# Performance work log

Hardware: AMD Instinct MI355X
Metric: run time of the kernel (lower is better)

The kernel has to match this reference:

```python
import jax, jax.numpy as jnp
import numpy as np

B, L = 1024, 50
H = 512
N_ITEM, N_ENTITY, N_WORD = 50000, 100000, 30000


def setup_inputs() -> dict:
    key = jax.random.key(0)
    ks = jax.random.split(key, 16)
    inp = {
        "item_ids": jax.random.randint(ks[0], (B, L), 0, N_ITEM),
        "item_len": jax.random.randint(ks[1], (B,), 0, 51),
        "entity_ids": jax.random.randint(ks[2], (B, L), 0, N_ENTITY),
        "entity_len": jax.random.randint(ks[3], (B,), 0, 51),
        "word_ids": jax.random.randint(ks[4], (B, L), 0, N_WORD),
        "word_len": jax.random.randint(ks[5], (B,), 0, 51),
        "labels": jax.random.randint(ks[6], (B,), 0, N_ITEM),
        # learned parameters (torch default-ish init scales)
        "item_emb": jax.random.normal(ks[7], (N_ITEM, H), jnp.float32),
        "entity_emb": jax.random.normal(ks[8], (N_ENTITY, H), jnp.float32),
        "word_emb": jax.random.normal(ks[9], (N_WORD, H), jnp.float32),
        "W1": jax.random.normal(ks[10], (H, 4 * H), jnp.float32) / np.sqrt(H),
        "b1": jnp.zeros((4 * H,), jnp.float32),
        "W2": jax.random.normal(ks[11], (4 * H, N_ITEM), jnp.float32) / np.sqrt(4 * H),
        "b2": jnp.zeros((N_ITEM,), jnp.float32),
    }
    return inp


def _masked_mean(table, ids, lens):
    # segment-mean over ragged lists encoded as padded ids + lengths.
    # empty list -> zeros (matches the torch zero-fallback branch).
    mask = (jnp.arange(L)[None, :] < lens[:, None]).astype(table.dtype)  # [B,L]
    emb = table[ids]                                                     # [B,L,H]
    s = jnp.einsum("blh,bl->bh", emb, mask)
    denom = jnp.maximum(lens, 1).astype(table.dtype)[:, None]
    return s / denom


def reference(item_emb, entity_emb, word_emb, W1, b1, W2, b2,
              item_ids, item_len, entity_ids, entity_len,
              word_ids, word_len, labels):
    u = (_masked_mean(item_emb, item_ids, item_len)
         + _masked_mean(entity_emb, entity_ids, entity_len)
         + _masked_mean(word_emb, word_ids, word_len)) / 3.0   # [B,H]
    h = jax.nn.relu(u @ W1 + b1)                                # [B,4H]
    probs = jax.nn.softmax(h @ W2 + b2, axis=-1)                # [B,n_item]
    # faithful to source: CrossEntropyLoss applied on top of softmax outputs
    logp = jax.nn.log_softmax(probs, axis=-1)
    loss = -jnp.mean(jnp.take_along_axis(logp, labels[:, None], axis=-1))
    return probs, labels, loss
```

## Files before the change

### kernel.cpp

```cpp
#include <hip/hip_runtime.h>
#include <cstdint>
#include <cstddef>

typedef __attribute__((ext_vector_type(8))) short bf16x8;
typedef __attribute__((ext_vector_type(4))) float f32x4;

#define B_DIM 1024
#define L_SEQ 50
#define H_DIM 512
#define NITEM 50000
#define PSTRIDE 400

__device__ __forceinline__ unsigned short f2bf(float x) {
  unsigned u = __float_as_uint(x);
  return (unsigned short)((u + 0x7fffu + ((u >> 16) & 1u)) >> 16);
}
__device__ __forceinline__ unsigned pack2(float lo, float hi) {
  return (unsigned)f2bf(lo) | ((unsigned)f2bf(hi) << 16);
}

__global__ void mean_kernel(const int* __restrict__ item_ids, const int* __restrict__ item_len,
                            const int* __restrict__ ent_ids, const int* __restrict__ ent_len,
                            const int* __restrict__ word_ids, const int* __restrict__ word_len,
                            const float* __restrict__ item_emb, const float* __restrict__ ent_emb,
                            const float* __restrict__ word_emb, unsigned short* __restrict__ u_bf) {
  const int b = blockIdx.x >> 1;
  const int col = ((blockIdx.x & 1) << 8) + threadIdx.x;
  float out = 0.f;
  {
    const int len = item_len[b]; float a = 0.f;
#pragma unroll 4
    for (int l = 0; l < len; ++l) a += item_emb[(size_t)item_ids[b * L_SEQ + l] * H_DIM + col];
    out += a / (float)(len > 0 ? len : 1);
  }
  {
    const int len = ent_len[b]; float a = 0.f;
#pragma unroll 4
    for (int l = 0; l < len; ++l) a += ent_emb[(size_t)ent_ids[b * L_SEQ + l] * H_DIM + col];
    out += a / (float)(len > 0 ? len : 1);
  }
  {
    const int len = word_len[b]; float a = 0.f;
#pragma unroll 4
    for (int l = 0; l < len; ++l) a += word_emb[(size_t)word_ids[b * L_SEQ + l] * H_DIM + col];
    out += a / (float)(len > 0 ? len : 1);
  }
  u_bf[b * H_DIM + col] = f2bf(out / 3.f);
}

template <int K, int N, int EPI>
__global__ __launch_bounds__(512, 2) void gemm_fused(const unsigned short* __restrict__ Ag,
                                                     const float* __restrict__ Bg,
                                                     const float* __restrict__ bias,
                                                     unsigned short* __restrict__ Cbf,
                                                     float* __restrict__ Cf,
                                                     float* __restrict__ pmax,
                                                     float* __restrict__ psum) {
  __shared__ unsigned short As[2][256 * 64];
  __shared__ uint4 Bs[2][8 * 128];

  const int tid = threadIdx.x;
  const int lane = tid & 63;
  const int wid = tid >> 6;
  const int m0 = blockIdx.x * 256;
  const int n0 = blockIdx.y * 128;

  const int arow = tid >> 3;
  const int ach = tid & 7;
  const int bn = 2 * lane;
  const int bk = 8 * wid;
  const int bcolg = (n0 + bn < N - 2) ? (n0 + bn) : (N - 2);

  uint4 areg[4];
  float2 breg[8];
  f32x4 acc[4][4] = {};

  auto stage_global = [&](int kt) {
    const int k0 = kt * 64;
#pragma unroll
    for (int q = 0; q < 4; ++q)
      areg[q] = *(const uint4*)&Ag[(size_t)(m0 + arow + 64 * q) * K + k0 + 8 * ach];
#pragma unroll
    for (int i = 0; i < 8; ++i)
      breg[i] = *(const float2*)&Bg[(size_t)(k0 + bk + i) * N + bcolg];
  };

  auto stage_lds = [&](int buf) {
#pragma unroll
    for (int q = 0; q < 4; ++q) {
      const int row = arow + 64 * q;
      *(uint4*)&As[buf][row * 64 + ((8 * ach) ^ ((row & 7) * 8))] = areg[q];
    }
    uint4 c0, c1;
    c0.x = pack2(breg[0].x, breg[1].x); c0.y = pack2(breg[2].x, breg[3].x);
    c0.z = pack2(breg[4].x, breg[5].x); c0.w = pack2(breg[6].x, breg[7].x);
    c1.x = pack2(breg[0].y, breg[1].y); c1.y = pack2(breg[2].y, breg[3].y);
    c1.z = pack2(breg[4].y, breg[5].y); c1.w = pack2(breg[6].y, breg[7].y);
    Bs[buf][wid * 128 + bn] = c0;
    Bs[buf][wid * 128 + bn + 1] = c1;
  };

  const int wr = wid & 3, wc = wid >> 2;
  const int mw = 64 * wr, nw = 64 * wc;
  const int l15 = lane & 15, kb = lane >> 4;

  auto compute = [&](int buf) {
#pragma unroll
    for (int koi = 0; koi < 2; ++koi) {
      bf16x8 af[4], bfv[4];
#pragma unroll
      for (int i = 0; i < 4; ++i) {
        const int row = mw + 16 * i + l15;
        af[i] = *(const bf16x8*)&As[buf][row * 64 + ((32 * koi + 8 * kb) ^ ((row & 7) * 8))];
      }
#pragma unroll
      for (int j = 0; j < 4; ++j)
        bfv[j] = *(const bf16x8*)&Bs[buf][(4 * koi + kb) * 128 + nw + 16 * j + l15];
#pragma unroll
      for (int i = 0; i < 4; ++i)
#pragma unroll
        for (int j = 0; j < 4; ++j)
          acc[i][j] = __builtin_amdgcn_mfma_f32_16x16x32_bf16(af[i], bfv[j], acc[i][j], 0, 0, 0);
    }
  };

  const int NT = K / 64;
  stage_global(0);
  stage_lds(0);
  __syncthreads();
  for (int t = 0; t < NT; ++t) {
    const int cur = t & 1;
    if (t + 1 < NT) stage_global(t + 1);
    compute(cur);
    if (t + 1 < NT) stage_lds(cur ^ 1);
    __syncthreads();
  }

  float bv[4];
  bool val[4];
#pragma unroll
  for (int j = 0; j < 4; ++j) {
    const int cg = n0 + nw + 16 * j + l15;
    val[j] = (cg < N);
    bv[j] = bias[val[j] ? cg : 0];
  }
#pragma unroll
  for (int i = 0; i < 4; ++i) {
    const int rbase = m0 + mw + 16 * i + 4 * kb;
#pragma unroll
    for (int j = 0; j < 4; ++j) {
      if (val[j]) {
        const int cg = n0 + nw + 16 * j + l15;
#pragma unroll
        for (int r = 0; r < 4; ++r) {
          const float v = acc[i][j][r] + bv[j];
          if (EPI == 0)
            Cbf[(size_t)(rbase + r) * N + cg] = f2bf(v > 0.f ? v : 0.f);
          else
            Cf[(size_t)(rbase + r) * N + cg] = v;
        }
      }
    }
  }

  if constexpr (EPI == 1) {
    float* redm = (float*)&As[0][0];
    float* reds = redm + 512;
#pragma unroll
    for (int i = 0; i < 4; ++i) {
#pragma unroll
      for (int r = 0; r < 4; ++r) {
        float mx = -3.0e38f;
#pragma unroll
        for (int j = 0; j < 4; ++j)
          if (val[j]) mx = fmaxf(mx, acc[i][j][r] + bv[j]);
#pragma unroll
        for (int d = 1; d < 16; d <<= 1) mx = fmaxf(mx, __shfl_xor(mx, d));
        float s = 0.f;
#pragma unroll
        for (int j = 0; j < 4; ++j)
          if (val[j]) s += expf(acc[i][j][r] + bv[j] - mx);
#pragma unroll
        for (int d = 1; d < 16; d <<= 1) s += __shfl_xor(s, d);
        if (l15 == 0) {
          const int rl = mw + 16 * i + 4 * kb + r;
          redm[wc * 256 + rl] = mx;
          reds[wc * 256 + rl] = s;
        }
      }
    }
    __syncthreads();
    if (tid < 256) {
      const float ma = redm[tid], mb = redm[256 + tid];
      const float mm = fmaxf(ma, mb);
      const float ss = reds[tid] * expf(ma - mm) + reds[256 + tid] * expf(mb - mm);
      pmax[(size_t)(m0 + tid) * PSTRIDE + blockIdx.y] = mm;
      psum[(size_t)(m0 + tid) * PSTRIDE + blockIdx.y] = ss;
    }
  }
}

__global__ void smax1r(const float* __restrict__ pmax, const float* __restrict__ psum,
                       float* __restrict__ rms, int ntiles) {
  const int b = blockIdx.x;
  const int l = threadIdx.x;
  float m = -3.4e38f, s = 0.f;
  for (int i = l; i < ntiles; i += 64) {
    const float pm = pmax[(size_t)b * PSTRIDE + i];
    const float ps = psum[(size_t)b * PSTRIDE + i];
    const float nm = fmaxf(m, pm);
    s = s * expf(m - nm) + ps * expf(pm - nm);
    m = nm;
  }
  for (int d = 1; d < 64; d <<= 1) {
    const float om = __shfl_xor(m, d), os = __shfl_xor(s, d);
    const float nm = fmaxf(m, om);
    s = s * expf(m - nm) + os * expf(om - nm);
    m = nm;
  }
  if (l == 0) {
    rms[b] = m;
    rms[B_DIM + b] = s;
  }
}

__global__ void smax2(float* __restrict__ buf, const float* __restrict__ rms,
                      const int* __restrict__ labels, float* __restrict__ row_lp) {
  const int b = blockIdx.x;
  float4* p = (float4*)(buf + (size_t)b * NITEM);
  const float m = rms[b];
  const float inv = 1.f / rms[B_DIM + b];
  const int lab = labels[b];
  __shared__ float s_pl;
  __shared__ float ss[256];
  float s2 = 0.f;
  for (int i = threadIdx.x; i < NITEM / 4; i += 256) {
    const float4 v = p[i];
    float pr[4];
#pragma unroll
    for (int j = 0; j < 4; ++j) {
      pr[j] = expf((&v.x)[j] - m) * inv;
      s2 += expf(pr[j] - inv);
    }
    float4 w;
    w.x = pr[0]; w.y = pr[1]; w.z = pr[2]; w.w = pr[3];
    p[i] = w;
    if ((lab >> 2) == i) s_pl = pr[lab & 3];
  }
  ss[threadIdx.x] = s2;
  __syncthreads();
  for (int off = 128; off > 0; off >>= 1) {
    if (threadIdx.x < off) ss[threadIdx.x] += ss[threadIdx.x + off];
    __syncthreads();
  }
  if (threadIdx.x == 0) row_lp[b] = s_pl - (inv + logf(ss[0]));
}

__global__ void fin(const float* __restrict__ row_lp, const int* __restrict__ labels,
                    float* __restrict__ out) {
  __shared__ float sb[256];
  float a = 0.f;
  for (int i = threadIdx.x; i < B_DIM; i += 256) {
    a += row_lp[i];
    out[(size_t)B_DIM * NITEM + i] = (float)labels[i];
  }
  sb[threadIdx.x] = a;
  __syncthreads();
  for (int off = 128; off > 0; off >>= 1) {
    if (threadIdx.x < off) sb[threadIdx.x] += sb[threadIdx.x + off];
    __syncthreads();
  }
  if (threadIdx.x == 0) out[(size_t)B_DIM * NITEM + B_DIM] = -sb[0] / (float)B_DIM;
}

extern "C" void kernel_launch(void* const* d_in, const int* in_sizes, int n_in,
                              void* d_out, int out_size, void* d_ws, size_t ws_size,
                              hipStream_t stream) {
  const int* item_ids = (const int*)d_in[0];
  const int* item_len = (const int*)d_in[1];
  const int* ent_ids = (const int*)d_in[2];
  const int* ent_len = (const int*)d_in[3];
  const int* word_ids = (const int*)d_in[4];
  const int* word_len = (const int*)d_in[5];
  const int* labels = (const int*)d_in[6];
  const float* item_emb = (const float*)d_in[7];
  const float* ent_emb = (const float*)d_in[8];
  const float* word_emb = (const float*)d_in[9];
  const float* W1 = (const float*)d_in[10];
  const float* b1 = (const float*)d_in[11];
  const float* W2 = (const float*)d_in[12];
  const float* b2 = (const float*)d_in[13];

  float* out = (float*)d_out;
  char* ws = (char*)d_ws;
  unsigned short* u_bf = (unsigned short*)ws;
  unsigned short* h_bf = (unsigned short*)(ws + (1 << 20));
  float* pmax = (float*)(ws + 5 * (1 << 20));
  float* psum = (float*)(ws + 7 * (1 << 20));
  float* rms = (float*)(ws + 9 * (1 << 20));
  float* row_lp = rms + 2 * B_DIM;
  float* logits = out;

  mean_kernel<<<2 * B_DIM, 256, 0, stream>>>(item_ids, item_len, ent_ids, ent_len, word_ids,
                                             word_len, item_emb, ent_emb, word_emb, u_bf);
  gemm_fused<512, 2048, 0><<<dim3(4, 16), 512, 0, stream>>>(u_bf, W1, b1, h_bf, nullptr,
                                                            nullptr, nullptr);
  gemm_fused<2048, 50000, 1><<<dim3(4, 391), 512, 0, stream>>>(h_bf, W2, b2, nullptr, logits,
                                                               pmax, psum);
  smax1r<<<B_DIM, 64, 0, stream>>>(pmax, psum, rms, 391);
  smax2<<<B_DIM, 256, 0, stream>>>(logits, rms, labels, row_lp);
  fin<<<1, 256, 0, stream>>>(row_lp, labels, out);
}
```

Baseline: 699.3 us.

## Pre-transpose weights to bf16 and use async LDS-load GEMM with 4-stage pipeline

Adds a kernel that transposes and converts W1/W2 from fp32 to bf16 K-major layout each call. A new GEMM streams tiles with global_load_lds into a 4-deep LDS ring, uses 256x256 tiles with an XCD-aware block remap and raised MFMA priority. It aims to halve weight bytes read by the main GEMM and to overlap loads with MFMA. In exchange it adds a full extra read of W2 (fp32) plus a bf16 write each call. The fast path runs only if the workspace is large enough.

Result: faster. 587.8 us (-15.9%).

```diff
diff --git a/kernel.cpp b/kernel.cpp
--- a/kernel.cpp
+++ b/kernel.cpp
@@ -17,6 +17,10 @@
 }
 __device__ __forceinline__ unsigned pack2(float lo, float hi) {
   return (unsigned)f2bf(lo) | ((unsigned)f2bf(hi) << 16);
+}
+__device__ __forceinline__ void gld16(const unsigned short* g, unsigned short* l) {
+  __builtin_amdgcn_global_load_lds((const __attribute__((address_space(1))) void*)g,
+                                   (__attribute__((address_space(3))) void*)l, 16, 0, 0);
 }
 
 __global__ void mean_kernel(const int* __restrict__ item_ids, const int* __restrict__ item_len,
@@ -48,6 +52,193 @@
   u_bf[b * H_DIM + col] = f2bf(out / 3.f);
 }
 
+template <int K, int N>
+__global__ void transpose_bf16(const float* __restrict__ W, unsigned short* __restrict__ Wt) {
+  __shared__ float tile[64][65];
+  const int k0 = blockIdx.x * 64, n0 = blockIdx.y * 64;
+  const int tn = threadIdx.x & 63, tk = threadIdx.x >> 6;
+  const int nv = (n0 + tn < N) ? n0 + tn : N - 1;
+#pragma unroll
+  for (int i = 0; i < 16; ++i)
+    tile[tk + 4 * i][tn] = W[(size_t)(k0 + tk + 4 * i) * N + nv];
+  __syncthreads();
+  const int rn = threadIdx.x >> 2, ck = (threadIdx.x & 3) * 16;
+  if (n0 + rn < N) {
+    uint4 o[2];
+    unsigned* po = (unsigned*)&o[0];
+#pragma unroll
+    for (int c = 0; c < 8; ++c)
+      po[c] = pack2(tile[ck + 2 * c][rn], tile[ck + 2 * c + 1][rn]);
+    *(uint4*)&Wt[(size_t)(n0 + rn) * K + k0 + ck] = o[0];
+    *(uint4*)&Wt[(size_t)(n0 + rn) * K + k0 + ck + 8] = o[1];
+  }
+}
+
+template <int K, int N, int EPI>
+__global__ __launch_bounds__(512, 2) void gemm_tt(const unsigned short* __restrict__ Ag,
+                                                  const unsigned short* __restrict__ Btg,
+                                                  const float* __restrict__ bias,
+                                                  unsigned short* __restrict__ Cbf,
+                                                  float* __restrict__ Cf,
+                                                  float* __restrict__ pmax,
+                                                  float* __restrict__ psum) {
+  __shared__ unsigned short lds[4][2][256 * 32];
+
+  const int tid = threadIdx.x;
+  const int lane = tid & 63;
+  const int wid = tid >> 6;
+
+  const int nwg = gridDim.x;
+  const int xcd = blockIdx.x & 7, off = blockIdx.x >> 3;
+  const int q = nwg >> 3, r = nwg & 7;
+  const int wgid = (xcd < r ? xcd * (q + 1) : r * (q + 1) + (xcd - r) * q) + off;
+  const int m0 = (wgid & 3) * 256;
+  const int bn = wgid >> 2;
+  const int n0 = bn * 256;
+
+  const int srow = wid * 16 + (lane >> 2);
+  const int schunk = lane & 3;
+  const unsigned short* pa[2];
+  const unsigned short* pb[2];
+  unsigned short* da[2];
+  unsigned short* db[2];
+#pragma unroll
+  for (int L = 0; L < 2; ++L) {
+    const int row = L * 128 + srow;
+    const int cg = schunk ^ ((row >> 1) & 3);
+    pa[L] = Ag + (size_t)(m0 + row) * K + cg * 8;
+    int rg = n0 + row;
+    rg = rg < N ? rg : N - 1;
+    pb[L] = Btg + (size_t)rg * K + cg * 8;
+    da[L] = &lds[0][0][L * 4096 + wid * 512];
+    db[L] = da[L] + 8192;
+  }
+
+  auto stage = [&](int t, int s) {
+    const int ko = t * 32;
+#pragma unroll
+    for (int L = 0; L < 2; ++L) gld16(pa[L] + ko, da[L] + s * 16384);
+#pragma unroll
+    for (int L = 0; L < 2; ++L) gld16(pb[L] + ko, db[L] + s * 16384);
+  };
+
+  const int wr = wid >> 2, wc = wid & 3;
+  const int l15 = lane & 15, kb = lane >> 4;
+  f32x4 acc[8][4] = {};
+
+  auto compute = [&](int s) {
+    bf16x8 af[8], bf[4];
+#pragma unroll
+    for (int i = 0; i < 8; ++i) {
+      const int row = wr * 128 + i * 16 + l15;
+      const int c = kb ^ ((row >> 1) & 3);
+      af[i] = *(const bf16x8*)&lds[s][0][row * 32 + c * 8];
+    }
+#pragma unroll
+    for (int j = 0; j < 4; ++j) {
+      const int col = wc * 64 + j * 16 + l15;
+      const int c = kb ^ ((col >> 1) & 3);
+      bf[j] = *(const bf16x8*)&lds[s][1][col * 32 + c * 8];
+    }
+    __builtin_amdgcn_s_setprio(1);
+#pragma unroll
+    for (int i = 0; i < 8; ++i)
+#pragma unroll
+      for (int j = 0; j < 4; ++j)
+        acc[i][j] = __builtin_amdgcn_mfma_f32_16x16x32_bf16(af[i], bf[j], acc[i][j], 0, 0, 0);
+    __builtin_amdgcn_s_setprio(0);
+  };
+
+  const int NT = K / 32;
+  stage(0, 0);
+  stage(1, 1);
+  asm volatile("s_waitcnt vmcnt(4)" ::: "memory");
+  __builtin_amdgcn_sched_barrier(0);
+  __builtin_amdgcn_s_barrier();
+  __builtin_amdgcn_sched_barrier(0);
+  for (int t = 0; t < NT; ++t) {
+    if (t + 2 < NT) stage(t + 2, (t + 2) & 3);
+    compute(t & 3);
+    if (t + 1 < NT) {
+      if (t + 2 < NT)
+        asm volatile("s_waitcnt vmcnt(4)" ::: "memory");
+      else
+        asm volatile("s_waitcnt vmcnt(0)" ::: "memory");
+      __builtin_amdgcn_sched_barrier(0);
+      __builtin_amdgcn_s_barrier();
+      __builtin_amdgcn_sched_barrier(0);
+    }
+  }
+
+  float bv[4];
+  bool val[4];
+#pragma unroll
+  for (int j = 0; j < 4; ++j) {
+    const int cg = n0 + wc * 64 + 16 * j + l15;
+    val[j] = (cg < N);
+    bv[j] = bias[val[j] ? cg : 0];
+  }
+#pragma unroll
+  for (int i = 0; i < 8; ++i) {
+    const int rbase = m0 + wr * 128 + 16 * i + 4 * kb;
+#pragma unroll
+    for (int j = 0; j < 4; ++j) {
+      if (val[j]) {
+        const int cg = n0 + wc * 64 + 16 * j + l15;
+#pragma unroll
+        for (int rr = 0; rr < 4; ++rr) {
+          const float v = acc[i][j][rr] + bv[j];
+          if (EPI == 0)
+            Cbf[(size_t)(rbase + rr) * N + cg] = f2bf(v > 0.f ? v : 0.f);
+          else
+            Cf[(size_t)(rbase + rr) * N + cg] = v;
+        }
+      }
+    }
+  }
+
+  if constexpr (EPI == 1) {
+    float* redm = (float*)&lds[0][0][0];
+    float* reds = redm + 1024;
+#pragma unroll
+    for (int i = 0; i < 8; ++i) {
+#pragma unroll
+      for (int rr = 0; rr < 4; ++rr) {
+        float mx = -3.0e38f;
+#pragma unroll
+        for (int j = 0; j < 4; ++j)
+          if (val[j]) mx = fmaxf(mx, acc[i][j][rr] + bv[j]);
+#pragma unroll
+        for (int d = 1; d < 16; d <<= 1) mx = fmaxf(mx, __shfl_xor(mx, d));
+        float s = 0.f;
+#pragma unroll
+        for (int j = 0; j < 4; ++j)
+          if (val[j]) s += expf(acc[i][j][rr] + bv[j] - mx);
+#pragma unroll
+        for (int d = 1; d < 16; d <<= 1) s += __shfl_xor(s, d);
+        if (l15 == 0) {
+          const int rw = wr * 128 + 16 * i + 4 * kb + rr;
+          redm[wc * 256 + rw] = mx;
+          reds[wc * 256 + rw] = s;
+        }
+      }
+    }
+    __syncthreads();
+    if (tid < 256) {
+      float mm = redm[tid], ss = reds[tid];
+#pragma unroll
+      for (int w = 1; w < 4; ++w) {
+        const float ma = redm[w * 256 + tid], sa = reds[w * 256 + tid];
+        const float nm = fmaxf(mm, ma);
+        ss = ss * expf(mm - nm) + sa * expf(ma - nm);
+        mm = nm;
+      }
+      pmax[(size_t)(m0 + tid) * PSTRIDE + bn] = mm;
+      psum[(size_t)(m0 + tid) * PSTRIDE + bn] = ss;
+    }
+  }
+}
+
 template <int K, int N, int EPI>
 __global__ __launch_bounds__(512, 2) void gemm_fused(const unsigned short* __restrict__ Ag,
                                                      const float* __restrict__ Bg,
@@ -58,38 +249,32 @@
                                                      float* __restrict__ psum) {
   __shared__ unsigned short As[2][256 * 64];
   __shared__ uint4 Bs[2][8 * 128];
-
   const int tid = threadIdx.x;
   const int lane = tid & 63;
   const int wid = tid >> 6;
   const int m0 = blockIdx.x * 256;
   const int n0 = blockIdx.y * 128;
-
   const int arow = tid >> 3;
   const int ach = tid & 7;
   const int bn = 2 * lane;
   const int bk = 8 * wid;
   const int bcolg = (n0 + bn < N - 2) ? (n0 + bn) : (N - 2);
-
   uint4 areg[4];
   float2 breg[8];
   f32x4 acc[4][4] = {};
-
   auto stage_global = [&](int kt) {
     const int k0 = kt * 64;
 #pragma unroll
-    for (int q = 0; q < 4; ++q)
-      areg[q] = *(const uint4*)&Ag[(size_t)(m0 + arow + 64 * q) * K + k0 + 8 * ach];
-#pragma unroll
-    for (int i = 0; i < 8; ++i)
-      breg[i] = *(const float2*)&Bg[(size_t)(k0 + bk + i) * N + bcolg];
+    for (int qq = 0; qq < 4; ++qq)
+      areg[qq] = *(const uint4*)&Ag[(size_t)(m0 + arow + 64 * qq) * K + k0 + 8 * ach];
+#pragma unroll
+    for (int i = 0; i < 8; ++i) breg[i] = *(const float2*)&Bg[(size_t)(k0 + bk + i) * N + bcolg];
   };
-
   auto stage_lds = [&](int buf) {
 #pragma unroll
-    for (int q = 0; q < 4; ++q) {
-      const int row = arow + 64 * q;
-      *(uint4*)&As[buf][row * 64 + ((8 * ach) ^ ((row & 7) * 8))] = areg[q];
+    for (int qq = 0; qq < 4; ++qq) {
+      const int row = arow + 64 * qq;
+      *(uint4*)&As[buf][row * 64 + ((8 * ach) ^ ((row & 7) * 8))] = areg[qq];
     }
     uint4 c0, c1;
     c0.x = pack2(breg[0].x, breg[1].x); c0.y = pack2(breg[2].x, breg[3].x);
@@ -99,11 +284,9 @@
     Bs[buf][wid * 128 + bn] = c0;
     Bs[buf][wid * 128 + bn + 1] = c1;
   };
-
   const int wr = wid & 3, wc = wid >> 2;
   const int mw = 64 * wr, nw = 64 * wc;
   const int l15 = lane & 15, kb = lane >> 4;
-
   auto compute = [&](int buf) {
 #pragma unroll
     for (int koi = 0; koi < 2; ++koi) {
@@ -123,7 +306,6 @@
           acc[i][j] = __builtin_amdgcn_mfma_f32_16x16x32_bf16(af[i], bfv[j], acc[i][j], 0, 0, 0);
     }
   };
-
   const int NT = K / 64;
   stage_global(0);
   stage_lds(0);
@@ -135,7 +317,6 @@
     if (t + 1 < NT) stage_lds(cur ^ 1);
     __syncthreads();
   }
-
   float bv[4];
   bool val[4];
 #pragma unroll
@@ -152,38 +333,37 @@
       if (val[j]) {
         const int cg = n0 + nw + 16 * j + l15;
 #pragma unroll
-        for (int r = 0; r < 4; ++r) {
-          const float v = acc[i][j][r] + bv[j];
+        for (int rr = 0; rr < 4; ++rr) {
+          const float v = acc[i][j][rr] + bv[j];
           if (EPI == 0)
-            Cbf[(size_t)(rbase + r) * N + cg] = f2bf(v > 0.f ? v : 0.f);
+            Cbf[(size_t)(rbase + rr) * N + cg] = f2bf(v > 0.f ? v : 0.f);
           else
-            Cf[(size_t)(rbase + r) * N + cg] = v;
+            Cf[(size_t)(rbase + rr) * N + cg] = v;
         }
       }
     }
   }
-
   if constexpr (EPI == 1) {
     float* redm = (float*)&As[0][0];
     float* reds = redm + 512;
 #pragma unroll
     for (int i = 0; i < 4; ++i) {
 #pragma unroll
-      for (int r = 0; r < 4; ++r) {
+      for (int rr = 0; rr < 4; ++rr) {
         float mx = -3.0e38f;
 #pragma unroll
         for (int j = 0; j < 4; ++j)
-          if (val[j]) mx = fmaxf(mx, acc[i][j][r] + bv[j]);
+          if (val[j]) mx = fmaxf(mx, acc[i][j][rr] + bv[j]);
 #pragma unroll
         for (int d = 1; d < 16; d <<= 1) mx = fmaxf(mx, __shfl_xor(mx, d));
         float s = 0.f;
 #pragma unroll
         for (int j = 0; j < 4; ++j)
-          if (val[j]) s += expf(acc[i][j][r] + bv[j] - mx);
+          if (val[j]) s += expf(acc[i][j][rr] + bv[j] - mx);
 #pragma unroll
         for (int d = 1; d < 16; d <<= 1) s += __shfl_xor(s, d);
         if (l15 == 0) {
-          const int rl = mw + 16 * i + 4 * kb + r;
+          const int rl = mw + 16 * i + 4 * kb + rr;
           redm[wc * 256 + rl] = mx;
           reds[wc * 256 + rl] = s;
         }
@@ -299,15 +479,30 @@
   float* psum = (float*)(ws + 7 * (1 << 20));
   float* rms = (float*)(ws + 9 * (1 << 20));
   float* row_lp = rms + 2 * B_DIM;
+  unsigned short* W1t = (unsigned short*)(ws + 10 * (1 << 20));
+  unsigned short* W2t = (unsigned short*)(ws + 16 * (1 << 20));
   float* logits = out;
+
+  const size_t need = (size_t)16 * (1 << 20) + (size_t)NITEM * 2048 * 2;
+  const bool fast = ws_size >= need;
 
   mean_kernel<<<2 * B_DIM, 256, 0, stream>>>(item_ids, item_len, ent_ids, ent_len, word_ids,
                                              word_len, item_emb, ent_emb, word_emb, u_bf);
-  gemm_fused<512, 2048, 0><<<dim3(4, 16), 512, 0, stream>>>(u_bf, W1, b1, h_bf, nullptr,
-                                                            nullptr, nullptr);
-  gemm_fused<2048, 50000, 1><<<dim3(4, 391), 512, 0, stream>>>(h_bf, W2, b2, nullptr, logits,
-                                                               pmax, psum);
-  smax1r<<<B_DIM, 64, 0, stream>>>(pmax, psum, rms, 391);
+  if (fast) {
+    transpose_bf16<512, 2048><<<dim3(8, 32), 256, 0, stream>>>(W1, W1t);
+    transpose_bf16<2048, NITEM><<<dim3(32, 782), 256, 0, stream>>>(W2, W2t);
+    gemm_tt<512, 2048, 0><<<4 * 8, 512, 0, stream>>>(u_bf, W1t, b1, h_bf, nullptr, nullptr,
+                                                     nullptr);
+    gemm_tt<2048, NITEM, 1><<<4 * 196, 512, 0, stream>>>(h_bf, W2t, b2, nullptr, logits, pmax,
+                                                         psum);
+    smax1r<<<B_DIM, 64, 0, stream>>>(pmax, psum, rms, 196);
+  } else {
+    gemm_fused<512, 2048, 0><<<dim3(4, 16), 512, 0, stream>>>(u_bf, W1, b1, h_bf, nullptr,
+                                                              nullptr, nullptr);
+    gemm_fused<2048, NITEM, 1><<<dim3(4, 391), 512, 0, stream>>>(h_bf, W2, b2, nullptr, logits,
+                                                                 pmax, psum);
+    smax1r<<<B_DIM, 64, 0, stream>>>(pmax, psum, rms, 391);
+  }
   smax2<<<B_DIM, 256, 0, stream>>>(logits, rms, labels, row_lp);
   fin<<<1, 256, 0, stream>>>(row_lp, labels, out);
 }
```
